# Kernel tuning notes

Measured on AMD Instinct MI355X. Metric: run time of the kernel, lower is better.

Reference implementation:

```python
import jax, jax.numpy as jnp
import numpy as np

N = 100000   # nodes
E = 1000000  # edges (before self-loops)
D_IN = 16
H, C = 2, 64  # heads, hidden per head
EPS = 1e-5    # BatchNorm eps
SLOPE = 0.2   # LeakyReLU negative slope (GATConv default)


def setup_inputs() -> dict:
    key = jax.random.key(0)
    ks = jax.random.split(key, 40)
    rn = lambda k, s, sc=0.1: jax.random.normal(k, s, jnp.float32) * sc
    inp = {}
    inp["x"] = jax.random.normal(ks[0], (N, D_IN), jnp.float32)
    inp["edge_index"] = jax.random.randint(ks[1], (2, E), 0, N)
    i = 2
    for l, din in ((1, D_IN), (2, C), (3, C)):
        inp[f"W{l}"] = rn(ks[i], (din, H * C)); i += 1
        inp[f"as{l}"] = rn(ks[i], (H, C)); i += 1
        inp[f"ad{l}"] = rn(ks[i], (H, C)); i += 1
        inp[f"b{l}"] = jnp.zeros((C,), jnp.float32)
        inp[f"g{l}"] = jnp.ones((C,), jnp.float32)   # BN gamma
        inp[f"be{l}"] = jnp.zeros((C,), jnp.float32) # BN beta
    inp["mW1"] = rn(ks[i], (C + 5, C)); i += 1
    inp["mb1"] = jnp.zeros((C,), jnp.float32)
    inp["mW2"] = rn(ks[i], (C, C)); i += 1
    inp["mb2"] = jnp.zeros((C,), jnp.float32)
    inp["pW"] = rn(ks[i], (C, 1)); i += 1
    inp["pb"] = jnp.zeros((1,), jnp.float32)
    inp["vW"] = rn(ks[i], (C, 1)); i += 1
    inp["vb"] = jnp.zeros((1,), jnp.float32)
    return inp


def gat(x, src, dst, W, att_s, att_d, bias):
    # GATConv, heads=H, concat=False (mean over heads). Messages flow src->dst.
    h = (x @ W).reshape(-1, H, C)               # [N,H,C]
    a_s = jnp.sum(h * att_s, -1)                # [N,H]
    a_d = jnp.sum(h * att_d, -1)                # [N,H]
    e = jax.nn.leaky_relu(a_s[src] + a_d[dst], SLOPE)  # [Etot,H]
    e = e - jax.ops.segment_max(e, dst, num_segments=N)[dst]
    ee = jnp.exp(e)
    alpha = ee / (jax.ops.segment_sum(ee, dst, num_segments=N)[dst] + 1e-16)
    msg = h[src] * alpha[:, :, None]            # [Etot,H,C]
    out = jax.ops.segment_sum(msg, dst, num_segments=N)  # [N,H,C]
    return out.mean(1) + bias                   # [N,C]


def bn(h, g, b):
    m = h.mean(0)
    v = jnp.mean((h - m) ** 2, 0)  # biased variance (torch BN normalization)
    return (h - m) * jax.lax.rsqrt(v + EPS) * g + b


def reference(x, edge_index, W1, as1, ad1, b1, g1, be1,
              W2, as2, ad2, b2, g2, be2, W3, as3, ad3, b3, g3, be3,
              mW1, mb1, mW2, mb2, pW, pb, vW, vb):
    loops = jnp.arange(N)
    src = jnp.concatenate([edge_index[0], loops])  # add_self_loops=True
    dst = jnp.concatenate([edge_index[1], loops])
    ctx = x[:, 9:14]  # context features [N,5]
    h = jax.nn.relu(bn(gat(x, src, dst, W1, as1, ad1, b1), g1, be1))
    h = jax.nn.relu(bn(gat(h, src, dst, W2, as2, ad2, b2), g2, be2))
    h = jax.nn.relu(bn(gat(h, src, dst, W3, as3, ad3, b3), g3, be3))
    # dropout is identity in eval reference
    h = jnp.concatenate([h, ctx], axis=1)          # [N, C+5]
    h = jax.nn.relu(h @ mW1 + mb1) @ mW2 + mb2     # MLP
    logits = (h @ pW + pb).squeeze(-1)             # [N]
    value = (h @ vW + vb).squeeze(-1)              # [N]
    return logits, value
```

## Files before the change

kernel.cpp:

```cpp
#include <hip/hip_runtime.h>
#include <hip/hip_fp16.h>


__device__ __forceinline__ float leaky(float x) { return x > 0.f ? x : 0.2f * x; }

typedef float f32x4 __attribute__((ext_vector_type(4)));
typedef _Float16 f16x8 __attribute__((ext_vector_type(8)));

#define BCAP 4096
#define NSL 256

__global__ void bucket_hist(const int* __restrict__ dst, int* __restrict__ bcnt, int E) {
  __shared__ int cnt[512];
  int t = threadIdx.x;
  cnt[t] = 0; cnt[t + 256] = 0;
  __syncthreads();
  for (int e = blockIdx.x * blockDim.x + t; e < E; e += gridDim.x * blockDim.x)
    atomicAdd(&cnt[dst[e] >> 8], 1);
  __syncthreads();
  for (int i = t; i < 512; i += 256)
    if (cnt[i]) atomicAdd(&bcnt[i], cnt[i]);
}

__global__ void bucket_scan(const int* __restrict__ bcnt, int* __restrict__ boff,
                            int* __restrict__ bcur, int nbk) {
  __shared__ int temp[512];
  int t = threadIdx.x;
  int v = (t < nbk) ? bcnt[t] : 0;
  temp[t] = v;
  __syncthreads();
  for (int off = 1; off < 512; off <<= 1) {
    int add = (t >= off) ? temp[t - off] : 0;
    __syncthreads();
    temp[t] += add;
    __syncthreads();
  }
  if (t < nbk) {
    int ex = temp[t] - v;
    boff[t] = ex;
    bcur[t] = ex;
  }
}

__global__ __launch_bounds__(256) void bin_scatter(
    const int* __restrict__ src, const int* __restrict__ dst,
    int* __restrict__ bcur, int2* __restrict__ ebuf, int E) {
  __shared__ int cnt[512];
  __shared__ int base[512];
  int t = threadIdx.x;
  int beg = blockIdx.x * 8192;
  int end = min(E, beg + 8192);
  cnt[t] = 0; cnt[t + 256] = 0;
  __syncthreads();
  for (int e = beg + t; e < end; e += 256)
    atomicAdd(&cnt[dst[e] >> 8], 1);
  __syncthreads();
  for (int i = t; i < 512; i += 256) {
    base[i] = cnt[i] ? atomicAdd(&bcur[i], cnt[i]) : 0;
    cnt[i] = 0;
  }
  __syncthreads();
  for (int e = beg + t; e < end; e += 256) {
    int d = dst[e];
    int bk = d >> 8;
    int off = atomicAdd(&cnt[bk], 1);
    ebuf[base[bk] + off] = make_int2(src[e], d);
  }
}

__global__ __launch_bounds__(256) void bucket_sort(
    const int2* __restrict__ ebuf, const int* __restrict__ boff,
    int* __restrict__ col, int* __restrict__ row_ptr, int E, int n, int nbk) {
  __shared__ int2 eds[BCAP];
  __shared__ int dcnt[256];
  __shared__ int dbase[256];
  __shared__ int dexcl[256];
  int b = blockIdx.x, t = threadIdx.x;
  int S = boff[b];
  int Eend = (b + 1 < nbk) ? boff[b + 1] : E;
  int cnt = min(Eend - S, BCAP);
  for (int i = t; i < cnt; i += 256) eds[i] = ebuf[S + i];
  dcnt[t] = 0;
  __syncthreads();
  for (int i = t; i < cnt; i += 256) atomicAdd(&dcnt[eds[i].y & 255], 1);
  __syncthreads();
  int v = dcnt[t];
  dbase[t] = v;
  __syncthreads();
  for (int off = 1; off < 256; off <<= 1) {
    int add = (t >= off) ? dbase[t - off] : 0;
    __syncthreads();
    dbase[t] += add;
    __syncthreads();
  }
  int excl = dbase[t] - v;
  int d = (b << 8) + t;
  if (d < n) row_ptr[d] = S + excl;
  if (b == nbk - 1 && t == 0) row_ptr[n] = E;
  dcnt[t] = 0;
  dexcl[t] = excl;
  __syncthreads();
  for (int i = t; i < cnt; i += 256) {
    int2 e = eds[i];
    int dl = e.y & 255;
    int off = atomicAdd(&dcnt[dl], 1);
    col[S + dexcl[dl] + off] = e.x;
  }
}

__global__ __launch_bounds__(256) void bn_stats(const float* __restrict__ h,
                                                float* __restrict__ stats, int n) {
  __shared__ float ssum[64], ssq[64];
  int t = threadIdx.x;
  if (t < 64) { ssum[t] = 0.f; ssq[t] = 0.f; }
  __syncthreads();
  const float4* h4 = (const float4*)h;
  size_t total4 = (size_t)n * 16;
  size_t stride = (size_t)gridDim.x * blockDim.x;
  int cbase = ((int)(((size_t)blockIdx.x * blockDim.x + t) & 15)) * 4;
  float s0 = 0.f, s1 = 0.f, s2 = 0.f, s3 = 0.f;
  float q0 = 0.f, q1 = 0.f, q2 = 0.f, q3 = 0.f;
  for (size_t i = (size_t)blockIdx.x * blockDim.x + t; i < total4; i += stride) {
    float4 v = h4[i];
    s0 += v.x; q0 = fmaf(v.x, v.x, q0);
    s1 += v.y; q1 = fmaf(v.y, v.y, q1);
    s2 += v.z; q2 = fmaf(v.z, v.z, q2);
    s3 += v.w; q3 = fmaf(v.w, v.w, q3);
  }
  atomicAdd(&ssum[cbase + 0], s0); atomicAdd(&ssq[cbase + 0], q0);
  atomicAdd(&ssum[cbase + 1], s1); atomicAdd(&ssq[cbase + 1], q1);
  atomicAdd(&ssum[cbase + 2], s2); atomicAdd(&ssq[cbase + 2], q2);
  atomicAdd(&ssum[cbase + 3], s3); atomicAdd(&ssq[cbase + 3], q3);
  __syncthreads();
  if (t < 64) {
    stats[blockIdx.x * 128 + t] = ssum[t];
    stats[blockIdx.x * 128 + 64 + t] = ssq[t];
  }
}

__global__ void bn_finalize(const float* __restrict__ stats, const float* __restrict__ g,
                            const float* __restrict__ be, float* __restrict__ scsh,
                            float inv_n) {
  __shared__ float red[128];
  int t = threadIdx.x;
  int c = t & 63;
  int off = (t >> 6) * 64;
  float acc = 0.f;
  for (int b = 0; b < NSL; b++) acc += stats[b * 128 + off + c];
  red[t] = acc;
  __syncthreads();
  if (t < 64) {
    float mean = red[t] * inv_n;
    float var = red[64 + t] * inv_n - mean * mean;
    float sc = rsqrtf(var + 1e-5f) * g[t];
    scsh[t] = sc;
    scsh[64 + t] = be[t] - mean * sc;
  }
}

template <int K, bool BN>
__global__ __launch_bounds__(256) void gat_project_mfma(
    const float* __restrict__ act, const float* __restrict__ scsh,
    const float* __restrict__ W,
    const float* __restrict__ att_s, const float* __restrict__ att_d,
    __half2* __restrict__ hb, float* __restrict__ as_,
    float* __restrict__ ad_, int n) {
  constexpr int KE = (K < 32) ? 32 : K;
  constexpr int KP = KE + 8;
  constexpr int STAGE = 64 * KP * 2 + 128 * KP * 2;
  constexpr int HSZ = 64 * 136 * 2;
  constexpr int LDSZ = (STAGE > HSZ) ? STAGE : HSZ;
  __shared__ __align__(16) char ldsb[LDSZ];
  __shared__ float attS[256];
  __half* aH = (__half*)ldsb;
  __half* wT = (__half*)(ldsb + 64 * KP * 2);
  __half* hS = (__half*)ldsb;

  int t = threadIdx.x;
  int node0 = blockIdx.x * 64;
  int rows = min(64, n - node0);

  constexpr int ACH = 64 * KE / 4;
  for (int i = t; i < ACH; i += 256) {
    int r = i / (KE / 4), kc = i % (KE / 4);
    float4 v = make_float4(0.f, 0.f, 0.f, 0.f);
    if (r < rows && kc * 4 < K)
      v = *(const float4*)&act[(size_t)(node0 + r) * K + kc * 4];
    if (BN) {
      float4 sc4 = *(const float4*)&scsh[kc * 4];
      float4 sh4 = *(const float4*)&scsh[64 + kc * 4];
      v.x = fmaxf(fmaf(v.x, sc4.x, sh4.x), 0.f);
      v.y = fmaxf(fmaf(v.y, sc4.y, sh4.y), 0.f);
      v.z = fmaxf(fmaf(v.z, sc4.z, sh4.z), 0.f);
      v.w = fmaxf(fmaf(v.w, sc4.w, sh4.w), 0.f);
    }
    __half2 h01 = __floats2half2_rn(v.x, v.y);
    __half2 h23 = __floats2half2_rn(v.z, v.w);
    uint2 pk = make_uint2(__builtin_bit_cast(unsigned, h01),
                          __builtin_bit_cast(unsigned, h23));
    *(uint2*)&aH[r * KP + kc * 4] = pk;
  }
  for (int i = t; i < KE * 128; i += 256) {
    int k = i >> 7, c = i & 127;
    float wv = (k < K) ? W[k * 128 + c] : 0.f;
    wT[c * KP + k] = __float2half(wv);
  }
  attS[t] = (t < 128) ? att_s[t] : att_d[t - 128];
  __syncthreads();

  int w = t >> 6, l = t & 63;
  int cl = l & 15, r4 = l >> 4;
  int w16 = w * 16;

  f32x4 acc[8] = {};
#pragma unroll
  for (int ks = 0; ks < KE / 32; ks++) {
    f16x8 av = *(const f16x8*)&aH[(w16 + cl) * KP + ks * 32 + r4 * 8];
#pragma unroll
    for (int ct = 0; ct < 8; ct++) {
      f16x8 bv = *(const f16x8*)&wT[(ct * 16 + cl) * KP + ks * 32 + r4 * 8];
      acc[ct] = __builtin_amdgcn_mfma_f32_16x16x32_f16(av, bv, acc[ct], 0, 0, 0);
    }
  }

  float ats[8], atd[8];
#pragma unroll
  for (int ct = 0; ct < 8; ct++) {
    ats[ct] = attS[ct * 16 + cl];
    atd[ct] = attS[128 + ct * 16 + cl];
  }
#pragma unroll
  for (int i = 0; i < 4; i++) {
    float s0 = 0.f, s1 = 0.f, d0 = 0.f, d1 = 0.f;
#pragma unroll
    for (int ct = 0; ct < 4; ct++) {
      s0 = fmaf(acc[ct][i], ats[ct], s0);
      d0 = fmaf(acc[ct][i], atd[ct], d0);
      s1 = fmaf(acc[ct + 4][i], ats[ct + 4], s1);
      d1 = fmaf(acc[ct + 4][i], atd[ct + 4], d1);
    }
#pragma unroll
    for (int off = 1; off < 16; off <<= 1) {
      s0 += __shfl_xor(s0, off); s1 += __shfl_xor(s1, off);
      d0 += __shfl_xor(d0, off); d1 += __shfl_xor(d1, off);
    }
    int rloc = w16 + r4 * 4 + i;
    if (rloc < rows) {
      int row = node0 + rloc;
      if (cl == 0) as_[row * 2] = s0;
      else if (cl == 1) as_[row * 2 + 1] = s1;
      else if (cl == 2) ad_[row * 2] = d0;
      else if (cl == 3) ad_[row * 2 + 1] = d1;
    }
  }

  __syncthreads();
#pragma unroll
  for (int ct = 0; ct < 8; ct++)
#pragma unroll
    for (int i = 0; i < 4; i++)
      hS[(w16 + r4 * 4 + i) * 136 + ct * 16 + cl] = __float2half(acc[ct][i]);
  __syncthreads();
#pragma unroll
  for (int it = 0; it < 4; it++) {
    int flat = t + it * 256;
    int nd = flat >> 4, ch = flat & 15;
    if (nd < rows)
      *(uint4*)((char*)hb + (((size_t)(node0 + nd)) << 8) + (ch << 4)) =
          *(const uint4*)((const char*)hS + nd * 272 + (ch << 4));
  }
}

__device__ __forceinline__ void fma8(float* a, float my, uint4 raw) {
  float2 f;
  f = __half22float2(__builtin_bit_cast(__half2, raw.x)); a[0] = fmaf(my, f.x, a[0]); a[1] = fmaf(my, f.y, a[1]);
  f = __half22float2(__builtin_bit_cast(__half2, raw.y)); a[2] = fmaf(my, f.x, a[2]); a[3] = fmaf(my, f.y, a[3]);
  f = __half22float2(__builtin_bit_cast(__half2, raw.z)); a[4] = fmaf(my, f.x, a[4]); a[5] = fmaf(my, f.y, a[5]);
  f = __half22float2(__builtin_bit_cast(__half2, raw.w)); a[6] = fmaf(my, f.x, a[6]); a[7] = fmaf(my, f.y, a[7]);
}

__global__ __launch_bounds__(256) void gat_aggregate(
    const __half2* __restrict__ hb,
    const float* __restrict__ as_, const float* __restrict__ ad_,
    const int* __restrict__ row_ptr, const int* __restrict__ col,
    const float* __restrict__ bias, float* __restrict__ out, int n) {
  int w = (int)((blockIdx.x * blockDim.x + threadIdx.x) >> 6);
  int lane = threadIdx.x & 63;
  int g = lane >> 4, q = lane & 15;
  int d = w * 4 + g;
  if (d >= n) return;
  int hidx = (q >= 8) ? 1 : 0;
  int beg = row_ptr[d], end = row_ptr[d + 1];
  const uint4* hb4 = (const uint4*)hb;

  float ad_my = ad_[d * 2 + hidx];

  float a[8] = {};
  float asv = as_[d * 2 + hidx];
  float my = __expf(leaky(asv + ad_my));
  uint4 raw = hb4[(size_t)d * 16 + q];
  fma8(a, my, raw);
  float dpart = my;

  int k = beg;
  for (; k + 3 < end; k += 4) {
    int s0 = col[k], s1 = col[k + 1], s2 = col[k + 2], s3 = col[k + 3];
    float e0 = as_[s0 * 2 + hidx];
    float e1 = as_[s1 * 2 + hidx];
    float e2 = as_[s2 * 2 + hidx];
    float e3 = as_[s3 * 2 + hidx];
    uint4 r0 = hb4[(size_t)s0 * 16 + q];
    uint4 r1 = hb4[(size_t)s1 * 16 + q];
    uint4 r2 = hb4[(size_t)s2 * 16 + q];
    uint4 r3 = hb4[(size_t)s3 * 16 + q];
    float m0 = __expf(leaky(e0 + ad_my));
    float m1 = __expf(leaky(e1 + ad_my));
    float m2 = __expf(leaky(e2 + ad_my));
    float m3 = __expf(leaky(e3 + ad_my));
    fma8(a, m0, r0); fma8(a, m1, r1); fma8(a, m2, r2); fma8(a, m3, r3);
    dpart += m0 + m1 + m2 + m3;
  }
  for (; k < end; k++) {
    int s = col[k];
    float e = as_[s * 2 + hidx];
    uint4 r = hb4[(size_t)s * 16 + q];
    float m = __expf(leaky(e + ad_my));
    fma8(a, m, r);
    dpart += m;
  }

  float b[8];
#pragma unroll
  for (int i = 0; i < 8; i++) b[i] = __shfl_xor(a[i], 8);
  float denO = __shfl_xor(dpart, 8);

  if (q < 8) {
    float rr0 = 1.f / (dpart + 1e-16f), rr1 = 1.f / (denO + 1e-16f);
    float4 bl = *(const float4*)&bias[q * 8];
    float4 bh = *(const float4*)&bias[q * 8 + 4];
    f32x4 o0, o1;
    o0.x = 0.5f * (a[0] * rr0 + b[0] * rr1) + bl.x;
    o0.y = 0.5f * (a[1] * rr0 + b[1] * rr1) + bl.y;
    o0.z = 0.5f * (a[2] * rr0 + b[2] * rr1) + bl.z;
    o0.w = 0.5f * (a[3] * rr0 + b[3] * rr1) + bl.w;
    o1.x = 0.5f * (a[4] * rr0 + b[4] * rr1) + bh.x;
    o1.y = 0.5f * (a[5] * rr0 + b[5] * rr1) + bh.y;
    o1.z = 0.5f * (a[6] * rr0 + b[6] * rr1) + bh.z;
    o1.w = 0.5f * (a[7] * rr0 + b[7] * rr1) + bh.w;
    f32x4* outp = (f32x4*)&out[(size_t)d * 64 + q * 8];
    __builtin_nontemporal_store(o0, outp);
    __builtin_nontemporal_store(o1, outp + 1);
  }
}

__global__ __launch_bounds__(256) void mlp_head_tiled(
    const float* __restrict__ h3raw, const float* __restrict__ scsh,
    const float* __restrict__ x,
    const float* __restrict__ mW1, const float* __restrict__ mb1,
    const float* __restrict__ mW2, const float* __restrict__ mb2,
    const float* __restrict__ pW, const float* __restrict__ pb,
    const float* __restrict__ vW, const float* __restrict__ vb,
    float* __restrict__ out, int n) {
  __shared__ float lds[9280];
  float* a1  = lds;
  float* ctx = lds + 4352;
  float* w1  = lds + 4864;

  int t = threadIdx.x;
  int node0 = blockIdx.x * 64;
  int rows = min(64, n - node0);

#pragma unroll
  for (int i = 0; i < 4; i++) {
    int flat = t + i * 256;
    int r = flat >> 4, kc = flat & 15;
    float4 v = make_float4(0.f, 0.f, 0.f, 0.f);
    if (r < rows) v = *(const float4*)&h3raw[(size_t)(node0 + r) * 64 + kc * 4];
    float4 sc4 = *(const float4*)&scsh[kc * 4];
    float4 sh4 = *(const float4*)&scsh[64 + kc * 4];
    v.x = fmaxf(fmaf(v.x, sc4.x, sh4.x), 0.f);
    v.y = fmaxf(fmaf(v.y, sc4.y, sh4.y), 0.f);
    v.z = fmaxf(fmaf(v.z, sc4.z, sh4.z), 0.f);
    v.w = fmaxf(fmaf(v.w, sc4.w, sh4.w), 0.f);
    *(float4*)&a1[r * 68 + kc * 4] = v;
  }
  for (int i = t; i < 320; i += 256) {
    int r = i / 5, j = i % 5;
    ctx[r * 8 + j] = (r < rows) ? x[(size_t)(node0 + r) * 16 + 9 + j] : 0.f;
  }
#pragma unroll
  for (int i = 0; i < 5; i++) {
    int flat = t + i * 256;
    if (flat < 1104) *(float4*)&w1[flat * 4] = *(const float4*)&mW1[flat * 4];
  }
  __syncthreads();

  int tc = t & 15, tr = t >> 4;
  int c0 = tc * 4, r0 = tr * 4;

  float acc[4][4] = {};
  for (int k = 0; k < 64; k += 4) {
    float4 av[4], wv[4];
#pragma unroll
    for (int i = 0; i < 4; i++) av[i] = *(const float4*)&a1[(r0 + i) * 68 + k];
#pragma unroll
    for (int j = 0; j < 4; j++) wv[j] = *(const float4*)&w1[(k + j) * 64 + c0];
#pragma unroll
    for (int i = 0; i < 4; i++) {
      const float* ai = (const float*)&av[i];
#pragma unroll
      for (int kk = 0; kk < 4; kk++) {
        const float* wr = (const float*)&wv[kk];
        acc[i][0] = fmaf(ai[kk], wr[0], acc[i][0]);
        acc[i][1] = fmaf(ai[kk], wr[1], acc[i][1]);
        acc[i][2] = fmaf(ai[kk], wr[2], acc[i][2]);
        acc[i][3] = fmaf(ai[kk], wr[3], acc[i][3]);
      }
    }
  }
#pragma unroll
  for (int k = 64; k < 69; k++) {
    float4 wv = *(const float4*)&w1[k * 64 + c0];
    const float* wr = (const float*)&wv;
#pragma unroll
    for (int i = 0; i < 4; i++) {
      float a = ctx[(r0 + i) * 8 + (k - 64)];
      acc[i][0] = fmaf(a, wr[0], acc[i][0]);
      acc[i][1] = fmaf(a, wr[1], acc[i][1]);
      acc[i][2] = fmaf(a, wr[2], acc[i][2]);
      acc[i][3] = fmaf(a, wr[3], acc[i][3]);
    }
  }
  float b1v0 = mb1[c0], b1v1 = mb1[c0 + 1], b1v2 = mb1[c0 + 2], b1v3 = mb1[c0 + 3];
  float4 t1v[4];
#pragma unroll
  for (int i = 0; i < 4; i++) {
    t1v[i].x = fmaxf(acc[i][0] + b1v0, 0.f);
    t1v[i].y = fmaxf(acc[i][1] + b1v1, 0.f);
    t1v[i].z = fmaxf(acc[i][2] + b1v2, 0.f);
    t1v[i].w = fmaxf(acc[i][3] + b1v3, 0.f);
  }
  __syncthreads();

#pragma unroll
  for (int i = 0; i < 4; i++)
    *(float4*)&a1[(r0 + i) * 68 + c0] = t1v[i];
#pragma unroll
  for (int i = 0; i < 4; i++) {
    int flat = t + i * 256;
    *(float4*)&w1[flat * 4] = *(const float4*)&mW2[flat * 4];
  }
  __syncthreads();

  float acc2[4][4] = {};
  for (int k = 0; k < 64; k += 4) {
    float4 av[4], wv[4];
#pragma unroll
    for (int i = 0; i < 4; i++) av[i] = *(const float4*)&a1[(r0 + i) * 68 + k];
#pragma unroll
    for (int j = 0; j < 4; j++) wv[j] = *(const float4*)&w1[(k + j) * 64 + c0];
#pragma unroll
    for (int i = 0; i < 4; i++) {
      const float* ai = (const float*)&av[i];
#pragma unroll
      for (int kk = 0; kk < 4; kk++) {
        const float* wr = (const float*)&wv[kk];
        acc2[i][0] = fmaf(ai[kk], wr[0], acc2[i][0]);
        acc2[i][1] = fmaf(ai[kk], wr[1], acc2[i][1]);
        acc2[i][2] = fmaf(ai[kk], wr[2], acc2[i][2]);
        acc2[i][3] = fmaf(ai[kk], wr[3], acc2[i][3]);
      }
    }
  }

  float b2v[4], pwv[4], vwv[4];
#pragma unroll
  for (int j = 0; j < 4; j++) {
    b2v[j] = mb2[c0 + j];
    pwv[j] = pW[c0 + j];
    vwv[j] = vW[c0 + j];
  }
  float p[4], v[4];
#pragma unroll
  for (int i = 0; i < 4; i++) {
    float ps = 0.f, vs = 0.f;
#pragma unroll
    for (int j = 0; j < 4; j++) {
      float u = acc2[i][j] + b2v[j];
      ps = fmaf(u, pwv[j], ps);
      vs = fmaf(u, vwv[j], vs);
    }
    p[i] = ps; v[i] = vs;
  }
#pragma unroll
  for (int off = 1; off < 16; off <<= 1) {
#pragma unroll
    for (int i = 0; i < 4; i++) {
      p[i] += __shfl_xor(p[i], off);
      v[i] += __shfl_xor(v[i], off);
    }
  }
  if (tc == 0) {
    float pbs = pb[0], vbs = vb[0];
#pragma unroll
    for (int i = 0; i < 4; i++) {
      int r = r0 + i;
      if (r < rows) {
        out[node0 + r] = p[i] + pbs;
        out[n + node0 + r] = v[i] + vbs;
      }
    }
  }
}

extern "C" void kernel_launch(void* const* d_in, const int* in_sizes, int n_in,
                              void* d_out, int out_size, void* d_ws, size_t ws_size,
                              hipStream_t stream) {
  const float* x = (const float*)d_in[0];
  const int* ei = (const int*)d_in[1];
  const float* W[3]  = {(const float*)d_in[2],  (const float*)d_in[8],  (const float*)d_in[14]};
  const float* AS[3] = {(const float*)d_in[3],  (const float*)d_in[9],  (const float*)d_in[15]};
  const float* AD[3] = {(const float*)d_in[4],  (const float*)d_in[10], (const float*)d_in[16]};
  const float* B[3]  = {(const float*)d_in[5],  (const float*)d_in[11], (const float*)d_in[17]};
  const float* G[3]  = {(const float*)d_in[6],  (const float*)d_in[12], (const float*)d_in[18]};
  const float* BE[3] = {(const float*)d_in[7],  (const float*)d_in[13], (const float*)d_in[19]};
  const float* mW1 = (const float*)d_in[20];
  const float* mb1 = (const float*)d_in[21];
  const float* mW2 = (const float*)d_in[22];
  const float* mb2 = (const float*)d_in[23];
  const float* pW  = (const float*)d_in[24];
  const float* pb  = (const float*)d_in[25];
  const float* vW  = (const float*)d_in[26];
  const float* vb  = (const float*)d_in[27];

  const int N = in_sizes[0] / 16;
  const int E = in_sizes[1] / 2;
  const int* srcp = ei;
  const int* dstp = ei + E;

  float* bufB  = (float*)d_ws;
  float* hbuf  = bufB + (size_t)N * 64;
  float* as_   = hbuf + (size_t)N * 64;
  float* ad_   = as_ + (size_t)N * 2;
  float* stats = ad_ + (size_t)N * 2;
  float* scsh  = stats + NSL * 128;
  int* row_ptr = (int*)(scsh + 128);
  int* bcnt    = row_ptr + (N + 1);
  int* boff    = bcnt + 512;
  int* bcur    = boff + 512;
  int* col     = bcur + 512;
  int2* ebuf   = (int2*)(col + E);
  __half2* hb  = (__half2*)hbuf;

  const int nbk = (N + 255) >> 8;
  const float inv_n = 1.0f / (float)N;

  hipMemsetAsync(bcnt, 0, sizeof(int) * 512, stream);
  bucket_hist<<<256, 256, 0, stream>>>(dstp, bcnt, E);
  bucket_scan<<<1, 512, 0, stream>>>(bcnt, boff, bcur, nbk);
  bin_scatter<<<(E + 8191) / 8192, 256, 0, stream>>>(srcp, dstp, bcur, ebuf, E);
  bucket_sort<<<nbk, 256, 0, stream>>>(ebuf, boff, col, row_ptr, E, N, nbk);

  const int tiles = (N + 63) / 64;
  const int agg_blocks = (N + 15) / 16;

  for (int l = 0; l < 3; l++) {
    if (l == 0)
      gat_project_mfma<16, false><<<tiles, 256, 0, stream>>>(x, scsh, W[l], AS[l], AD[l],
                                                             hb, as_, ad_, N);
    else
      gat_project_mfma<64, true><<<tiles, 256, 0, stream>>>(bufB, scsh, W[l], AS[l], AD[l],
                                                            hb, as_, ad_, N);
    gat_aggregate<<<agg_blocks, 256, 0, stream>>>(hb, as_, ad_, row_ptr, col,
                                                  B[l], bufB, N);
    bn_stats<<<NSL, 256, 0, stream>>>(bufB, stats, N);
    bn_finalize<<<1, 128, 0, stream>>>(stats, G[l], BE[l], scsh, inv_n);
  }

  mlp_head_tiled<<<tiles, 256, 0, stream>>>(bufB, scsh, x, mW1, mb1, mW2, mb2,
                                            pW, pb, vW, vb, (float*)d_out, N);
}
```

Baseline: 463.5 us.

## Fold attention vectors into projection weights and pre-transpose weights once

Adds a one-time kernel that converts all three layers' weights to fp16 in transposed layout and appends four extra columns holding W·att_s and W·att_d per head, so the attention logits come from a ninth MFMA tile instead of per-row dot products and shuffle reductions. Each projection block now copies the pre-transposed weights with vector loads rather than transposing scalar fp32 weights. bn_finalize is widened to 1024 threads so the reduction over 256 partial slices is split across more threads. The attention scores are now computed from fp16-rounded folded weights, which changes their rounding slightly.

```diff
diff --git a/kernel.cpp b/kernel.cpp
--- a/kernel.cpp
+++ b/kernel.cpp
@@ -108,6 +108,36 @@
   }
 }
 
+__global__ void transpose_ws(
+    const float* __restrict__ W0, const float* __restrict__ W1,
+    const float* __restrict__ W2,
+    const float* __restrict__ as0, const float* __restrict__ ad0,
+    const float* __restrict__ as1, const float* __restrict__ ad1,
+    const float* __restrict__ as2, const float* __restrict__ ad2,
+    __half* __restrict__ wTg) {
+  int i = blockIdx.x * 256 + threadIdx.x;
+  const float *W, *as, *ad;
+  int KE, K, j;
+  if (i < 4608)       { W = W0; as = as0; ad = ad0; KE = 32; K = 16; j = i; }
+  else if (i < 13824) { W = W1; as = as1; ad = ad1; KE = 64; K = 64; j = i - 4608; }
+  else if (i < 23040) { W = W2; as = as2; ad = ad2; KE = 64; K = 64; j = i - 13824; }
+  else return;
+  int r = j / KE, k = j % KE;
+  float v = 0.f;
+  if (k < K) {
+    if (r < 128) {
+      v = W[k * 128 + r];
+    } else if (r < 132) {
+      const float* att = (r & 2) ? ad : as;
+      int h = r & 1;
+      float acc = 0.f;
+      for (int c = 0; c < 64; c++) acc += W[k * 128 + h * 64 + c] * att[h * 64 + c];
+      v = acc;
+    }
+  }
+  wTg[i] = __float2half(v);
+}
+
 __global__ __launch_bounds__(256) void bn_stats(const float* __restrict__ h,
                                                 float* __restrict__ stats, int n) {
   __shared__ float ssum[64], ssq[64];
@@ -138,16 +168,23 @@
   }
 }
 
-__global__ void bn_finalize(const float* __restrict__ stats, const float* __restrict__ g,
-                            const float* __restrict__ be, float* __restrict__ scsh,
-                            float inv_n) {
-  __shared__ float red[128];
+__global__ __launch_bounds__(1024) void bn_finalize(
+    const float* __restrict__ stats, const float* __restrict__ g,
+    const float* __restrict__ be, float* __restrict__ scsh, float inv_n) {
+  __shared__ float red[1024];
   int t = threadIdx.x;
-  int c = t & 63;
-  int off = (t >> 6) * 64;
+  int c = t & 127;
+  int grp = t >> 7;
   float acc = 0.f;
-  for (int b = 0; b < NSL; b++) acc += stats[b * 128 + off + c];
+  for (int b = grp; b < NSL; b += 8) acc += stats[b * 128 + c];
   red[t] = acc;
+  __syncthreads();
+  if (t < 128) {
+    float s = red[t];
+#pragma unroll
+    for (int j = 1; j < 8; j++) s += red[t + 128 * j];
+    red[t] = s;
+  }
   __syncthreads();
   if (t < 64) {
     float mean = red[t] * inv_n;
@@ -161,17 +198,15 @@
 template <int K, bool BN>
 __global__ __launch_bounds__(256) void gat_project_mfma(
     const float* __restrict__ act, const float* __restrict__ scsh,
-    const float* __restrict__ W,
-    const float* __restrict__ att_s, const float* __restrict__ att_d,
+    const __half* __restrict__ wTg,
     __half2* __restrict__ hb, float* __restrict__ as_,
     float* __restrict__ ad_, int n) {
   constexpr int KE = (K < 32) ? 32 : K;
   constexpr int KP = KE + 8;
-  constexpr int STAGE = 64 * KP * 2 + 128 * KP * 2;
+  constexpr int STAGE = 64 * KP * 2 + 144 * KP * 2;
   constexpr int HSZ = 64 * 136 * 2;
   constexpr int LDSZ = (STAGE > HSZ) ? STAGE : HSZ;
   __shared__ __align__(16) char ldsb[LDSZ];
-  __shared__ float attS[256];
   __half* aH = (__half*)ldsb;
   __half* wT = (__half*)(ldsb + 64 * KP * 2);
   __half* hS = (__half*)ldsb;
@@ -200,57 +235,38 @@
                           __builtin_bit_cast(unsigned, h23));
     *(uint2*)&aH[r * KP + kc * 4] = pk;
   }
-  for (int i = t; i < KE * 128; i += 256) {
-    int k = i >> 7, c = i & 127;
-    float wv = (k < K) ? W[k * 128 + c] : 0.f;
-    wT[c * KP + k] = __float2half(wv);
-  }
-  attS[t] = (t < 128) ? att_s[t] : att_d[t - 128];
+  constexpr int WCH = 144 * KE / 8;
+  for (int i = t; i < WCH; i += 256) {
+    int c = i / (KE / 8), j = i % (KE / 8);
+    *(uint4*)&wT[c * KP + j * 8] = *(const uint4*)&wTg[c * KE + j * 8];
+  }
   __syncthreads();
 
   int w = t >> 6, l = t & 63;
   int cl = l & 15, r4 = l >> 4;
   int w16 = w * 16;
 
-  f32x4 acc[8] = {};
+  f32x4 acc[9] = {};
 #pragma unroll
   for (int ks = 0; ks < KE / 32; ks++) {
     f16x8 av = *(const f16x8*)&aH[(w16 + cl) * KP + ks * 32 + r4 * 8];
 #pragma unroll
-    for (int ct = 0; ct < 8; ct++) {
+    for (int ct = 0; ct < 9; ct++) {
       f16x8 bv = *(const f16x8*)&wT[(ct * 16 + cl) * KP + ks * 32 + r4 * 8];
       acc[ct] = __builtin_amdgcn_mfma_f32_16x16x32_f16(av, bv, acc[ct], 0, 0, 0);
     }
   }
 
-  float ats[8], atd[8];
-#pragma unroll
-  for (int ct = 0; ct < 8; ct++) {
-    ats[ct] = attS[ct * 16 + cl];
-    atd[ct] = attS[128 + ct * 16 + cl];
-  }
 #pragma unroll
   for (int i = 0; i < 4; i++) {
-    float s0 = 0.f, s1 = 0.f, d0 = 0.f, d1 = 0.f;
-#pragma unroll
-    for (int ct = 0; ct < 4; ct++) {
-      s0 = fmaf(acc[ct][i], ats[ct], s0);
-      d0 = fmaf(acc[ct][i], atd[ct], d0);
-      s1 = fmaf(acc[ct + 4][i], ats[ct + 4], s1);
-      d1 = fmaf(acc[ct + 4][i], atd[ct + 4], d1);
-    }
-#pragma unroll
-    for (int off = 1; off < 16; off <<= 1) {
-      s0 += __shfl_xor(s0, off); s1 += __shfl_xor(s1, off);
-      d0 += __shfl_xor(d0, off); d1 += __shfl_xor(d1, off);
-    }
     int rloc = w16 + r4 * 4 + i;
-    if (rloc < rows) {
+    if (rloc < rows && cl < 4) {
       int row = node0 + rloc;
-      if (cl == 0) as_[row * 2] = s0;
-      else if (cl == 1) as_[row * 2 + 1] = s1;
-      else if (cl == 2) ad_[row * 2] = d0;
-      else if (cl == 3) ad_[row * 2 + 1] = d1;
+      float sv = acc[8][i];
+      if (cl == 0) as_[row * 2] = sv;
+      else if (cl == 1) as_[row * 2 + 1] = sv;
+      else if (cl == 2) ad_[row * 2] = sv;
+      else ad_[row * 2 + 1] = sv;
     }
   }
 
@@ -544,17 +560,21 @@
   float* ad_   = as_ + (size_t)N * 2;
   float* stats = ad_ + (size_t)N * 2;
   float* scsh  = stats + NSL * 128;
-  int* row_ptr = (int*)(scsh + 128);
+  __half* wTg  = (__half*)(scsh + 128);
+  int* row_ptr = (int*)(wTg + 23040);
   int* bcnt    = row_ptr + (N + 1);
   int* boff    = bcnt + 512;
   int* bcur    = boff + 512;
   int* col     = bcur + 512;
   int2* ebuf   = (int2*)(col + E);
   __half2* hb  = (__half2*)hbuf;
+  const __half* wTgL[3] = {wTg, wTg + 4608, wTg + 13824};
 
   const int nbk = (N + 255) >> 8;
   const float inv_n = 1.0f / (float)N;
 
+  transpose_ws<<<90, 256, 0, stream>>>(W[0], W[1], W[2], AS[0], AD[0],
+                                       AS[1], AD[1], AS[2], AD[2], wTg);
   hipMemsetAsync(bcnt, 0, sizeof(int) * 512, stream);
   bucket_hist<<<256, 256, 0, stream>>>(dstp, bcnt, E);
   bucket_scan<<<1, 512, 0, stream>>>(bcnt, boff, bcur, nbk);
@@ -566,15 +586,15 @@
 
   for (int l = 0; l < 3; l++) {
     if (l == 0)
-      gat_project_mfma<16, false><<<tiles, 256, 0, stream>>>(x, scsh, W[l], AS[l], AD[l],
+      gat_project_mfma<16, false><<<tiles, 256, 0, stream>>>(x, scsh, wTgL[l],
                                                              hb, as_, ad_, N);
     else
-      gat_project_mfma<64, true><<<tiles, 256, 0, stream>>>(bufB, scsh, W[l], AS[l], AD[l],
+      gat_project_mfma<64, true><<<tiles, 256, 0, stream>>>(bufB, scsh, wTgL[l],
                                                             hb, as_, ad_, N);
     gat_aggregate<<<agg_blocks, 256, 0, stream>>>(hb, as_, ad_, row_ptr, col,
                                                   B[l], bufB, N);
     bn_stats<<<NSL, 256, 0, stream>>>(bufB, stats, N);
-    bn_finalize<<<1, 128, 0, stream>>>(stats, G[l], BE[l], scsh, inv_n);
+    bn_finalize<<<1, 1024, 0, stream>>>(stats, G[l], BE[l], scsh, inv_n);
   }
 
   mlp_head_tiled<<<tiles, 256, 0, stream>>>(bufB, scsh, x, mW1, mb1, mW2, mb2,
```

New measurement: 452.7 us. 2.3% less time.
